# Kernel optimization log

Measured on AMD Instinct MI355X. Metric: run time of the kernel, lower is better.

## Reference

```python
import jax, jax.numpy as jnp
import numpy as np

T = 8          # num_timesteps
H = 8          # num_heads
D = 128        # lifting_dim
ROPE_BASE = 10000.0


def apply_time_only_rope(x, num_nodes, num_timesteps, base=ROPE_BASE):
    # x: [B, H, num_nodes*num_timesteps, d_head], time-major flattening
    B, Hh, S, dh = x.shape
    half = dh // 2
    times = jnp.arange(num_timesteps, dtype=jnp.float32)
    freqs = 1.0 / base ** (2.0 * jnp.arange(half, dtype=jnp.float32) / dh)
    angle = times[:, None] * freqs[None, :]                 # [T, half]
    positions = jnp.repeat(jnp.arange(num_timesteps), num_nodes)  # [S]
    cos_g = jnp.cos(angle)[positions]                       # [S, half]
    sin_g = jnp.sin(angle)[positions]
    t1 = x[..., 0::2]
    t2 = x[..., 1::2]
    r0 = t1 * cos_g - t2 * sin_g
    r1 = t1 * sin_g + t2 * cos_g
    return jnp.stack([r0, r1], axis=-1).reshape(x.shape)


def setup_inputs() -> dict:
    key = jax.random.key(0)
    ks = jax.random.split(key, 16)
    B_T, N, E = 32, 2048, 8192
    inp = {
        'x_0': jax.random.normal(ks[0], (B_T, N, D), jnp.float32),
        'edge_attr': jax.random.normal(ks[1], (B_T, E, D), jnp.float32),
        'q_data': jax.random.normal(ks[2], (B_T, N, D), jnp.float32),
    }
    def lin(k):
        kw, kb = jax.random.split(k)
        return (jax.random.normal(kw, (D, D), jnp.float32) * 0.02,
                jax.random.normal(kb, (D,), jnp.float32) * 0.02)
    inp['Wq'], inp['bq'] = lin(ks[3])
    inp['Wk0'], inp['bk0'] = lin(ks[4])
    inp['Wv0'], inp['bv0'] = lin(ks[5])
    inp['Wk1'], inp['bk1'] = lin(ks[6])
    inp['Wv1'], inp['bv1'] = lin(ks[7])
    inp['Wo'], inp['bo'] = lin(ks[8])
    return inp


def reference(x_0, edge_attr, q_data, Wq, bq, Wk0, bk0, Wv0, bv0, Wk1, bk1, Wv1, bv1, Wo, bo):
    B_T, N, d = x_0.shape
    B = B_T // T
    dh = d // H

    def flatten_st(a):  # [B*T, M, d] -> [B, T*M, d]
        return a.reshape(B, T * a.shape[1], d)

    qf = flatten_st(q_data) @ Wq.T + bq                     # [B, T*N, d]
    q = qf.reshape(B, H, N * T, dh)                         # faithful torch .view
    q = jax.nn.softmax(q, axis=-1)
    q = apply_time_only_rope(q, N, T)

    out = q
    for (feat, Wk, bk, Wv, bv) in ((x_0, Wk0, bk0, Wv0, bv0),
                                   (edge_attr, Wk1, bk1, Wv1, bv1)):
        M = feat.shape[1]
        hf = flatten_st(feat)                               # [B, T*M, d]
        k = (hf @ Wk.T + bk).reshape(B, H, M * T, dh)
        v = (hf @ Wv.T + bv).reshape(B, H, M * T, dh)
        k = apply_time_only_rope(k, M, T)
        k = jax.nn.softmax(k, axis=-1)
        k_cumsum = k.sum(axis=-2, keepdims=True)            # [B,H,1,dh]
        D_inv = 1.0 / jnp.maximum((q * k_cumsum).sum(axis=-1, keepdims=True), 1e-8)
        kv = jnp.einsum('bhsd,bhse->bhde', k, v)            # [B,H,dh,dh]
        out = q + jnp.einsum('bhsd,bhde->bhse', q, kv) * D_inv

    out = out.transpose(0, 2, 1, 3).reshape(B, N * T, d)
    out = out @ Wo.T + bo
    return out.reshape(B * T, N, d)                         # unflatten_spatiotemporal
```

## Files before the change

kernel.cpp:

```cpp
#include <hip/hip_runtime.h>
#include <hip/hip_bf16.h>
#include <math.h>


typedef __attribute__((ext_vector_type(8))) short short8;
typedef __attribute__((ext_vector_type(4))) float float4v;

#define LN1E4_OVER8 1.1512925464970229f

#define OFF_QWS   0
#define OFF_FRG_Q 4194304
#define OFF_FRG_O 4202496
#define OFF_BFRG  4210688
#define OFF_KV    4227072
#define OFF_KCS   4235264
#define OFF_PART  4235776

__device__ __forceinline__ unsigned short f2bf(float f) {
    __hip_bfloat16 h = __float2bfloat16(f);
    return *reinterpret_cast<unsigned short*>(&h);
}
__device__ __forceinline__ float bf2f(unsigned short s) {
    return __uint_as_float(((unsigned)s) << 16);
}
__device__ __forceinline__ unsigned pk2(float a, float b) {
    __hip_bfloat162 h = __float22bfloat162_rn(make_float2(a, b));
    return *reinterpret_cast<unsigned*>(&h);
}
__device__ __forceinline__ float frcp(float x) {
    return __builtin_amdgcn_rcpf(x);
}
template<int C> __device__ __forceinline__ float dppadd(float x) {
    int r = __builtin_amdgcn_update_dpp(0, __float_as_int(x), C, 0xF, 0xF, true);
    return x + __int_as_float(r);
}
__device__ __forceinline__ float sum16(float x) {
    x = dppadd<0xB1>(x);
    x = dppadd<0x4E>(x);
    x = dppadd<0x141>(x);
    x = dppadd<0x140>(x);
    return x;
}
__device__ __forceinline__ float qperm1(float x) {
    int r = __builtin_amdgcn_update_dpp(0, __float_as_int(x), 0xB1, 0xF, 0xF, true);
    return __int_as_float(r);
}

__global__ void k_prep(const float* __restrict__ Wq, const float* __restrict__ Wk1,
                       const float* __restrict__ Wv1, const float* __restrict__ Wo,
                       float* __restrict__ ws) {
    int i = blockIdx.x * 256 + threadIdx.x;
    if (i < 32768) {
        int j = i & 16383;
        int jE = j & 7, lane = (j >> 3) & 63, km = (j >> 9) & 3, cg = j >> 11;
        int n = cg * 16 + (lane & 15);
        int kk = km * 32 + (lane >> 4) * 8 + jE;
        const float* W = (i < 16384) ? Wq : Wo;
        unsigned short* dst = (unsigned short*)(ws + ((i < 16384) ? OFF_FRG_Q : OFF_FRG_O));
        dst[j] = f2bf(W[n * 128 + kk]);
    } else if (i < 65536) {
        int j = i - 32768;
        int jE = j & 7, lane = (j >> 3) & 63, km = (j >> 9) & 3, cg = j >> 11;
        int n = cg * 16 + (lane & 15);
        int k = km * 32 + (lane >> 4) * 8 + jE;
        float w = (cg < 8) ? Wk1[n * 128 + k] : Wv1[(n - 128) * 128 + k];
        ((unsigned short*)(ws + OFF_BFRG))[j] = f2bf(w);
    } else {
        int j = i - 65536;
        if (j < 8704) ws[OFF_KV + j] = 0.f;
    }
}

__global__ __launch_bounds__(256, 4) void k_main(const float* __restrict__ ea,
                                                 const float* __restrict__ bk,
                                                 const float* __restrict__ bv,
                                                 const float* __restrict__ qd,
                                                 const float* __restrict__ bq,
                                                 float* __restrict__ ws) {
    __shared__ __align__(16) char smem[40960];
    int t = threadIdx.x;
    int wave = t >> 6, lane = t & 63, quad = lane >> 4, n = lane & 15;
    int g = blockIdx.x;

    if (g % 5 == 4) {
        int blk = g / 5;
        unsigned short* aT = (unsigned short*)smem;
        unsigned* qws32 = (unsigned*)(ws + OFF_QWS);
        long base = (long)blk * 128;
        int b = blk >> 7;
        int h = (blk & 127) >> 4;
        int s0 = (blk & 15) * 1024;
        int t1 = (blk & 15) >> 1;

        const short8* fq = (const short8*)((const unsigned short*)(ws + OFF_FRG_Q));
        short8 Bf[2][4];
        #pragma unroll
        for (int ct = 0; ct < 2; ++ct)
            #pragma unroll
            for (int km = 0; km < 4; ++km)
                Bf[ct][km] = fq[((2 * wave + ct) * 4 + km) * 64 + lane];

        #pragma unroll
        for (int i = 0; i < 16; ++i) {
            int idx = i * 256 + t;
            int row = idx >> 5, c4 = idx & 31;
            float4 v = ((const float4*)qd)[(base + row) * 32 + c4];
            unsigned short* p = aT + row * 128 + (((c4 >> 1) ^ (row & 7)) << 3) + (c4 & 1) * 4;
            *(uint2*)p = make_uint2(pk2(v.x, v.y), pk2(v.z, v.w));
        }
        __syncthreads();

        float fr = __expf(-LN1E4_OVER8 * (float)(n >> 1));
        float sa, ca; __sincosf((float)t1 * fr, &sa, &ca);
        float sgn = (n & 1) ? sa : -sa;
        float bias0 = bq[(2 * wave) * 16 + n];
        float bias1 = bq[(2 * wave + 1) * 16 + n];

        #pragma unroll
        for (int rt = 0; rt < 8; ++rt) {
            float4v a0 = (float4v){0.f, 0.f, 0.f, 0.f};
            float4v a1 = (float4v){0.f, 0.f, 0.f, 0.f};
            int row = rt * 16 + n;
            __builtin_amdgcn_s_setprio(1);
            #pragma unroll
            for (int km = 0; km < 4; ++km) {
                short8 Af = *(const short8*)(aT + row * 128 + (((km * 4 + quad) ^ (n & 7)) << 3));
                a0 = __builtin_amdgcn_mfma_f32_16x16x32_bf16(Af, Bf[0][km], a0, 0, 0, 0);
                a1 = __builtin_amdgcn_mfma_f32_16x16x32_bf16(Af, Bf[1][km], a1, 0, 0, 0);
            }
            __builtin_amdgcn_s_setprio(0);
            #pragma unroll
            for (int ct = 0; ct < 2; ++ct) {
                int cg = 2 * wave + ct;
                float bias = ct ? bias1 : bias0;
                float4v x = ct ? a1 : a0;
                #pragma unroll
                for (int i = 0; i < 4; ++i) {
                    float e = __expf(x[i] + bias);
                    float q = e * frcp(sum16(e));
                    float r = fmaf(qperm1(q), sgn, q * ca);
                    unsigned pkd = ((unsigned)f2bf(qperm1(r)) << 16) | (unsigned)f2bf(r);
                    if ((n & 1) == 0) {
                        int sp = s0 + (rt * 16 + quad * 4 + i) * 8 + cg;
                        long qoff = ((long)(b * 8 + h) * 16384 + sp) * 16 + n;
                        qws32[qoff >> 1] = pkd;
                    }
                }
            }
        }
        return;
    }

    int blk = g - g / 5;
    unsigned short* aT = (unsigned short*)smem;
    unsigned short* kbuf = (unsigned short*)(smem + 32768) + wave * 1024;
    unsigned short* vbuf = kbuf + 512;
    long base = (long)blk * 128;
    int sl = (blk & 511) << 7;
    int t2 = (sl & 8191) >> 10;

    #pragma unroll
    for (int i = 0; i < 16; ++i) {
        int idx = i * 256 + t;
        int row = idx >> 5, c4 = idx & 31;
        float4 v = ((const float4*)ea)[(base + row) * 32 + c4];
        unsigned short* p = aT + row * 128 + (((c4 >> 1) ^ (row & 7)) << 3) + (c4 & 1) * 4;
        *(uint2*)p = make_uint2(pk2(v.x, v.y), pk2(v.z, v.w));
    }

    const short8* bfrag = (const short8*)((const unsigned short*)(ws + OFF_BFRG));
    short8 Bf[4][4];
    #pragma unroll
    for (int ct = 0; ct < 4; ++ct) {
        int cg = (ct < 2) ? (2 * wave + ct) : (8 + 2 * wave + (ct - 2));
        #pragma unroll
        for (int km = 0; km < 4; ++km)
            Bf[ct][km] = bfrag[(cg * 4 + km) * 64 + lane];
    }

    float bias[4];
    #pragma unroll
    for (int ct = 0; ct < 4; ++ct)
        bias[ct] = (ct < 2) ? bk[(2 * wave + ct) * 16 + n] : bv[(2 * wave + ct - 2) * 16 + n];
    float fr = __expf(-LN1E4_OVER8 * (float)(n >> 1));
    float sv, cvv; __sincosf((float)t2 * fr, &sv, &cvv);
    float sgn = (n & 1) ? sv : -sv;
    float kcsacc = 0.f;
    float4v kvacc = (float4v){0.f, 0.f, 0.f, 0.f};

    __syncthreads();

    #pragma unroll
    for (int rt = 0; rt < 8; ++rt) {
        float4v acc[4];
        #pragma unroll
        for (int ct = 0; ct < 4; ++ct) acc[ct] = (float4v){0.f, 0.f, 0.f, 0.f};

        int row = rt * 16 + n;
        short8 Af[4];
        #pragma unroll
        for (int km = 0; km < 4; ++km)
            Af[km] = *(const short8*)(aT + row * 128 + (((km * 4 + quad) ^ (n & 7)) << 3));
        __builtin_amdgcn_s_setprio(1);
        #pragma unroll
        for (int ct = 0; ct < 4; ++ct)
            #pragma unroll
            for (int km = 0; km < 4; ++km)
                acc[ct] = __builtin_amdgcn_mfma_f32_16x16x32_bf16(Af[km], Bf[ct][km], acc[ct], 0, 0, 0);
        __builtin_amdgcn_s_setprio(0);

        #pragma unroll
        for (int ct = 0; ct < 4; ++ct) {
            float x0 = acc[ct][0] + bias[ct];
            float x1 = acc[ct][1] + bias[ct];
            float x2 = acc[ct][2] + bias[ct];
            float x3 = acc[ct][3] + bias[ct];
            if (ct < 2) {
                x0 = fmaf(qperm1(x0), sgn, x0 * cvv); x1 = fmaf(qperm1(x1), sgn, x1 * cvv);
                x2 = fmaf(qperm1(x2), sgn, x2 * cvv); x3 = fmaf(qperm1(x3), sgn, x3 * cvv);
                x0 = __expf(x0); x1 = __expf(x1); x2 = __expf(x2); x3 = __expf(x3);
                x0 *= frcp(sum16(x0)); x1 *= frcp(sum16(x1));
                x2 *= frcp(sum16(x2)); x3 *= frcp(sum16(x3));
                kcsacc += x0 + x1 + x2 + x3;
            }
            unsigned short* dst = (ct < 2) ? kbuf : vbuf;
            int o = (ct & 1) * 16 + quad * 4;
            *(uint2*)(dst + n * 32 + (((o >> 3) ^ (n & 3)) << 3) + (o & 7)) =
                make_uint2(pk2(x0, x1), pk2(x2, x3));
        }

        asm volatile("s_waitcnt lgkmcnt(0)" ::: "memory");
        __builtin_amdgcn_sched_barrier(0);

        {
            int off = ((quad ^ (n & 3)) << 3);
            short8 Ak = *(const short8*)(kbuf + n * 32 + off);
            short8 Bv = *(const short8*)(vbuf + n * 32 + off);
            kvacc = __builtin_amdgcn_mfma_f32_16x16x32_bf16(Ak, Bv, kvacc, 0, 0, 0);
        }
    }

    kcsacc += __shfl_xor(kcsacc, 16); kcsacc += __shfl_xor(kcsacc, 32);
    float* part = ws + OFF_PART + ((long)blk * 4 + wave) * 272;
    #pragma unroll
    for (int r = 0; r < 4; ++r) part[(quad * 4 + r) * 16 + n] = kvacc[r];
    if (lane < 16) part[256 + n] = kcsacc;
}

__global__ void k_red(float* __restrict__ ws) {
    int blk = blockIdx.x, t = threadIdx.x;
    if (t >= 272) return;
    int bh = blk >> 3, g = blk & 7;
    const float* part = ws + OFF_PART + (long)bh * 256 * 272 + (long)g * 32 * 272 + t;
    float s = 0.f;
    #pragma unroll 8
    for (int i = 0; i < 32; ++i) s += part[(long)i * 272];
    float* dst = (t < 256) ? (ws + OFF_KV + bh * 256 + t)
                           : (ws + OFF_KCS + bh * 16 + (t - 256));
    atomicAdd(dst, s);
}

__global__ __launch_bounds__(256, 4) void k_out(const float* __restrict__ bo,
                                                float* __restrict__ ws,
                                                float* __restrict__ out) {
    __shared__ __align__(16) unsigned short tile[64 * 128];
    const unsigned short* qws16 = (const unsigned short*)(ws + OFF_QWS);
    int t = threadIdx.x, blk = blockIdx.x;
    int wave = t >> 6, lane = t & 63, quad = lane >> 4, n = lane & 15;
    int b = blk >> 8;
    int sp0 = (blk & 255) * 64;

    #pragma unroll
    for (int i = 0; i < 8; ++i) {
        int idx = i * 256 + t;
        int h = idx >> 8, rr = (idx >> 2) & 63, seg = idx & 3;
        uint2 u = *(const uint2*)(qws16 + ((long)(b * 8 + h) * 16384 + sp0 + rr) * 16 + seg * 4);
        unsigned short* p = tile + rr * 128 + (((h * 2 + (seg >> 1)) ^ (rr & 7)) << 3) + (seg & 1) * 4;
        *(uint2*)p = u;
    }

    short8 Bkv[2], Bden[2];
    #pragma unroll
    for (int ct = 0; ct < 2; ++ct) {
        int h = 2 * wave + ct;
        const float* kvp = ws + OFF_KV + (b * 8 + h) * 256;
        const float* ksp = ws + OFF_KCS + (b * 8 + h) * 16;
        short8 bk8 = {0, 0, 0, 0, 0, 0, 0, 0}, bd8 = {0, 0, 0, 0, 0, 0, 0, 0};
        bool act = (ct == 0) ? (quad < 2) : (quad >= 2);
        int kbase = (ct == 0) ? quad * 8 : (quad - 2) * 8;
        if (act) {
            #pragma unroll
            for (int jj = 0; jj < 8; ++jj) {
                bk8[jj] = (short)f2bf(kvp[(kbase + jj) * 16 + n]);
                bd8[jj] = (short)f2bf(ksp[kbase + jj]);
            }
        }
        Bkv[ct] = bk8; Bden[ct] = bd8;
    }
    const short8* fo = (const short8*)((const unsigned short*)(ws + OFF_FRG_O));
    short8 Bo[2][4];
    #pragma unroll
    for (int ct = 0; ct < 2; ++ct)
        #pragma unroll
        for (int km = 0; km < 4; ++km)
            Bo[ct][km] = fo[((2 * wave + ct) * 4 + km) * 64 + lane];
    __syncthreads();

    #pragma unroll
    for (int pass = 0; pass < 2; ++pass) {
        unsigned short fh[2][2][4];
        #pragma unroll
        for (int rtl = 0; rtl < 2; ++rtl) {
            int rt = pass * 2 + rtl;
            int row = rt * 16 + n;
            short8 Af = *(const short8*)(tile + row * 128 + (((wave * 4 + quad) ^ (n & 7)) << 3));
            float4v P0 = __builtin_amdgcn_mfma_f32_16x16x32_bf16(Af, Bkv[0], (float4v){0.f,0.f,0.f,0.f}, 0, 0, 0);
            float4v P1 = __builtin_amdgcn_mfma_f32_16x16x32_bf16(Af, Bkv[1], (float4v){0.f,0.f,0.f,0.f}, 0, 0, 0);
            float4v D0 = __builtin_amdgcn_mfma_f32_16x16x32_bf16(Af, Bden[0], (float4v){0.f,0.f,0.f,0.f}, 0, 0, 0);
            float4v D1 = __builtin_amdgcn_mfma_f32_16x16x32_bf16(Af, Bden[1], (float4v){0.f,0.f,0.f,0.f}, 0, 0, 0);
            #pragma unroll
            for (int ct = 0; ct < 2; ++ct) {
                int cg = 2 * wave + ct;
                float4v P = ct ? P1 : P0;
                float4v D = ct ? D1 : D0;
                #pragma unroll
                for (int i = 0; i < 4; ++i) {
                    int rw = rt * 16 + quad * 4 + i;
                    int col = cg * 16 + n;
                    float qv = bf2f(tile[rw * 128 + (((col >> 3) ^ (rw & 7)) << 3) + (col & 7)]);
                    float inv = frcp(fmaxf(D[i], 1e-8f));
                    fh[rtl][ct][i] = f2bf(fmaf(P[i], inv, qv));
                }
            }
        }
        __syncthreads();
        #pragma unroll
        for (int rtl = 0; rtl < 2; ++rtl)
            #pragma unroll
            for (int ct = 0; ct < 2; ++ct) {
                int cg = 2 * wave + ct;
                #pragma unroll
                for (int i = 0; i < 4; ++i) {
                    int rw = (pass * 2 + rtl) * 16 + quad * 4 + i;
                    int col = cg * 16 + n;
                    tile[rw * 128 + (((col >> 3) ^ (rw & 7)) << 3) + (col & 7)] = fh[rtl][ct][i];
                }
            }
    }
    __syncthreads();

    float bb0 = bo[(2 * wave) * 16 + n];
    float bb1 = bo[(2 * wave + 1) * 16 + n];
    #pragma unroll
    for (int rt = 0; rt < 4; ++rt) {
        float4v a0 = (float4v){0.f, 0.f, 0.f, 0.f};
        float4v a1 = (float4v){0.f, 0.f, 0.f, 0.f};
        int row = rt * 16 + n;
        #pragma unroll
        for (int km = 0; km < 4; ++km) {
            short8 Af = *(const short8*)(tile + row * 128 + (((km * 4 + quad) ^ (n & 7)) << 3));
            a0 = __builtin_amdgcn_mfma_f32_16x16x32_bf16(Af, Bo[0][km], a0, 0, 0, 0);
            a1 = __builtin_amdgcn_mfma_f32_16x16x32_bf16(Af, Bo[1][km], a1, 0, 0, 0);
        }
        #pragma unroll
        for (int ct = 0; ct < 2; ++ct) {
            int cg = 2 * wave + ct;
            float bb = ct ? bb1 : bb0;
            float4v a = ct ? a1 : a0;
            #pragma unroll
            for (int i = 0; i < 4; ++i) {
                float v = a[i] + bb;
                float pv = qperm1(v);
                if ((n & 1) == 0) {
                    long rg = (long)b * 16384 + sp0 + rt * 16 + quad * 4 + i;
                    *(float2*)(out + rg * 128 + cg * 16 + n) = make_float2(v, pv);
                }
            }
        }
    }
}

extern "C" void kernel_launch(void* const* d_in, const int* in_sizes, int n_in,
                              void* d_out, int out_size, void* d_ws, size_t ws_size,
                              hipStream_t stream) {
    (void)in_sizes; (void)n_in; (void)out_size; (void)ws_size;
    const float* edge = (const float*)d_in[1];
    const float* qd   = (const float*)d_in[2];
    const float* Wq   = (const float*)d_in[3];
    const float* bq   = (const float*)d_in[4];
    const float* Wk1  = (const float*)d_in[9];
    const float* bk1  = (const float*)d_in[10];
    const float* Wv1  = (const float*)d_in[11];
    const float* bv1  = (const float*)d_in[12];
    const float* Wo   = (const float*)d_in[13];
    const float* bo   = (const float*)d_in[14];
    float* ws  = (float*)d_ws;
    float* out = (float*)d_out;

    hipLaunchKernelGGL(k_prep, dim3(290),  dim3(256), 0, stream, Wq, Wk1, Wv1, Wo, ws);
    hipLaunchKernelGGL(k_main, dim3(2560), dim3(256), 0, stream, edge, bk1, bv1, qd, bq, ws);
    hipLaunchKernelGGL(k_red,  dim3(256),  dim3(320), 0, stream, ws);
    hipLaunchKernelGGL(k_out,  dim3(1024), dim3(256), 0, stream, bo, ws, out);
}
```

Before: 283.0 us.

## Halve k_main LDS tile for higher occupancy, widen k_red, load Q directly in k_out

k_main now stages its 128-row input in two 64-row halves, which cuts shared memory from 40KB to 24KB and raises the launch-bounds occupancy target from 4 to 6 blocks. k_red doubles its grid so each block sums 16 partials instead of 32. k_out no longer stages Q into LDS first: it reads MFMA A-fragments and the residual q values straight from global memory, and it drops the per-pass barrier. In exchange there is an extra barrier per half in k_main, register pressure is tighter under the higher occupancy bound, and k_out does more scattered global reads and issues more atomics.

```diff
diff --git a/kernel.cpp b/kernel.cpp
--- a/kernel.cpp
+++ b/kernel.cpp
@@ -71,13 +71,13 @@
     }
 }
 
-__global__ __launch_bounds__(256, 4) void k_main(const float* __restrict__ ea,
+__global__ __launch_bounds__(256, 6) void k_main(const float* __restrict__ ea,
                                                  const float* __restrict__ bk,
                                                  const float* __restrict__ bv,
                                                  const float* __restrict__ qd,
                                                  const float* __restrict__ bq,
                                                  float* __restrict__ ws) {
-    __shared__ __align__(16) char smem[40960];
+    __shared__ __align__(16) char smem[24576];
     int t = threadIdx.x;
     int wave = t >> 6, lane = t & 63, quad = lane >> 4, n = lane & 15;
     int g = blockIdx.x;
@@ -100,16 +100,6 @@
             for (int km = 0; km < 4; ++km)
                 Bf[ct][km] = fq[((2 * wave + ct) * 4 + km) * 64 + lane];
 
-        #pragma unroll
-        for (int i = 0; i < 16; ++i) {
-            int idx = i * 256 + t;
-            int row = idx >> 5, c4 = idx & 31;
-            float4 v = ((const float4*)qd)[(base + row) * 32 + c4];
-            unsigned short* p = aT + row * 128 + (((c4 >> 1) ^ (row & 7)) << 3) + (c4 & 1) * 4;
-            *(uint2*)p = make_uint2(pk2(v.x, v.y), pk2(v.z, v.w));
-        }
-        __syncthreads();
-
         float fr = __expf(-LN1E4_OVER8 * (float)(n >> 1));
         float sa, ca; __sincosf((float)t1 * fr, &sa, &ca);
         float sgn = (n & 1) ? sa : -sa;
@@ -117,33 +107,48 @@
         float bias1 = bq[(2 * wave + 1) * 16 + n];
 
         #pragma unroll
-        for (int rt = 0; rt < 8; ++rt) {
-            float4v a0 = (float4v){0.f, 0.f, 0.f, 0.f};
-            float4v a1 = (float4v){0.f, 0.f, 0.f, 0.f};
-            int row = rt * 16 + n;
-            __builtin_amdgcn_s_setprio(1);
-            #pragma unroll
-            for (int km = 0; km < 4; ++km) {
-                short8 Af = *(const short8*)(aT + row * 128 + (((km * 4 + quad) ^ (n & 7)) << 3));
-                a0 = __builtin_amdgcn_mfma_f32_16x16x32_bf16(Af, Bf[0][km], a0, 0, 0, 0);
-                a1 = __builtin_amdgcn_mfma_f32_16x16x32_bf16(Af, Bf[1][km], a1, 0, 0, 0);
-            }
-            __builtin_amdgcn_s_setprio(0);
-            #pragma unroll
-            for (int ct = 0; ct < 2; ++ct) {
-                int cg = 2 * wave + ct;
-                float bias = ct ? bias1 : bias0;
-                float4v x = ct ? a1 : a0;
+        for (int half = 0; half < 2; ++half) {
+            if (half) __syncthreads();
+            #pragma unroll
+            for (int i = 0; i < 8; ++i) {
+                int idx = i * 256 + t;
+                int row = idx >> 5, c4 = idx & 31;
+                float4 v = ((const float4*)qd)[(base + half * 64 + row) * 32 + c4];
+                unsigned short* p = aT + row * 128 + (((c4 >> 1) ^ (row & 7)) << 3) + (c4 & 1) * 4;
+                *(uint2*)p = make_uint2(pk2(v.x, v.y), pk2(v.z, v.w));
+            }
+            __syncthreads();
+
+            #pragma unroll
+            for (int rl = 0; rl < 4; ++rl) {
+                int rt = half * 4 + rl;
+                float4v a0 = (float4v){0.f, 0.f, 0.f, 0.f};
+                float4v a1 = (float4v){0.f, 0.f, 0.f, 0.f};
+                int row = rl * 16 + n;
+                __builtin_amdgcn_s_setprio(1);
                 #pragma unroll
-                for (int i = 0; i < 4; ++i) {
-                    float e = __expf(x[i] + bias);
-                    float q = e * frcp(sum16(e));
-                    float r = fmaf(qperm1(q), sgn, q * ca);
-                    unsigned pkd = ((unsigned)f2bf(qperm1(r)) << 16) | (unsigned)f2bf(r);
-                    if ((n & 1) == 0) {
-                        int sp = s0 + (rt * 16 + quad * 4 + i) * 8 + cg;
-                        long qoff = ((long)(b * 8 + h) * 16384 + sp) * 16 + n;
-                        qws32[qoff >> 1] = pkd;
+                for (int km = 0; km < 4; ++km) {
+                    short8 Af = *(const short8*)(aT + row * 128 + (((km * 4 + quad) ^ (n & 7)) << 3));
+                    a0 = __builtin_amdgcn_mfma_f32_16x16x32_bf16(Af, Bf[0][km], a0, 0, 0, 0);
+                    a1 = __builtin_amdgcn_mfma_f32_16x16x32_bf16(Af, Bf[1][km], a1, 0, 0, 0);
+                }
+                __builtin_amdgcn_s_setprio(0);
+                #pragma unroll
+                for (int ct = 0; ct < 2; ++ct) {
+                    int cg = 2 * wave + ct;
+                    float bias = ct ? bias1 : bias0;
+                    float4v x = ct ? a1 : a0;
+                    #pragma unroll
+                    for (int i = 0; i < 4; ++i) {
+                        float e = __expf(x[i] + bias);
+                        float q = e * frcp(sum16(e));
+                        float r = fmaf(qperm1(q), sgn, q * ca);
+                        unsigned pkd = ((unsigned)f2bf(qperm1(r)) << 16) | (unsigned)f2bf(r);
+                        if ((n & 1) == 0) {
+                            int sp = s0 + (rt * 16 + quad * 4 + i) * 8 + cg;
+                            long qoff = ((long)(b * 8 + h) * 16384 + sp) * 16 + n;
+                            qws32[qoff >> 1] = pkd;
+                        }
                     }
                 }
             }
@@ -153,20 +158,11 @@
 
     int blk = g - g / 5;
     unsigned short* aT = (unsigned short*)smem;
-    unsigned short* kbuf = (unsigned short*)(smem + 32768) + wave * 1024;
+    unsigned short* kbuf = (unsigned short*)(smem + 16384) + wave * 1024;
     unsigned short* vbuf = kbuf + 512;
     long base = (long)blk * 128;
     int sl = (blk & 511) << 7;
     int t2 = (sl & 8191) >> 10;
-
-    #pragma unroll
-    for (int i = 0; i < 16; ++i) {
-        int idx = i * 256 + t;
-        int row = idx >> 5, c4 = idx & 31;
-        float4 v = ((const float4*)ea)[(base + row) * 32 + c4];
-        unsigned short* p = aT + row * 128 + (((c4 >> 1) ^ (row & 7)) << 3) + (c4 & 1) * 4;
-        *(uint2*)p = make_uint2(pk2(v.x, v.y), pk2(v.z, v.w));
-    }
 
     const short8* bfrag = (const short8*)((const unsigned short*)(ws + OFF_BFRG));
     short8 Bf[4][4];
@@ -188,55 +184,67 @@
     float kcsacc = 0.f;
     float4v kvacc = (float4v){0.f, 0.f, 0.f, 0.f};
 
-    __syncthreads();
-
-    #pragma unroll
-    for (int rt = 0; rt < 8; ++rt) {
-        float4v acc[4];
-        #pragma unroll
-        for (int ct = 0; ct < 4; ++ct) acc[ct] = (float4v){0.f, 0.f, 0.f, 0.f};
-
-        int row = rt * 16 + n;
-        short8 Af[4];
-        #pragma unroll
-        for (int km = 0; km < 4; ++km)
-            Af[km] = *(const short8*)(aT + row * 128 + (((km * 4 + quad) ^ (n & 7)) << 3));
-        __builtin_amdgcn_s_setprio(1);
-        #pragma unroll
-        for (int ct = 0; ct < 4; ++ct)
+    #pragma unroll
+    for (int half = 0; half < 2; ++half) {
+        if (half) __syncthreads();
+        #pragma unroll
+        for (int i = 0; i < 8; ++i) {
+            int idx = i * 256 + t;
+            int row = idx >> 5, c4 = idx & 31;
+            float4 v = ((const float4*)ea)[(base + half * 64 + row) * 32 + c4];
+            unsigned short* p = aT + row * 128 + (((c4 >> 1) ^ (row & 7)) << 3) + (c4 & 1) * 4;
+            *(uint2*)p = make_uint2(pk2(v.x, v.y), pk2(v.z, v.w));
+        }
+        __syncthreads();
+
+        #pragma unroll
+        for (int rl = 0; rl < 4; ++rl) {
+            float4v acc[4];
+            #pragma unroll
+            for (int ct = 0; ct < 4; ++ct) acc[ct] = (float4v){0.f, 0.f, 0.f, 0.f};
+
+            int row = rl * 16 + n;
+            short8 Af[4];
             #pragma unroll
             for (int km = 0; km < 4; ++km)
-                acc[ct] = __builtin_amdgcn_mfma_f32_16x16x32_bf16(Af[km], Bf[ct][km], acc[ct], 0, 0, 0);
-        __builtin_amdgcn_s_setprio(0);
-
-        #pragma unroll
-        for (int ct = 0; ct < 4; ++ct) {
-            float x0 = acc[ct][0] + bias[ct];
-            float x1 = acc[ct][1] + bias[ct];
-            float x2 = acc[ct][2] + bias[ct];
-            float x3 = acc[ct][3] + bias[ct];
-            if (ct < 2) {
-                x0 = fmaf(qperm1(x0), sgn, x0 * cvv); x1 = fmaf(qperm1(x1), sgn, x1 * cvv);
-                x2 = fmaf(qperm1(x2), sgn, x2 * cvv); x3 = fmaf(qperm1(x3), sgn, x3 * cvv);
-                x0 = __expf(x0); x1 = __expf(x1); x2 = __expf(x2); x3 = __expf(x3);
-                x0 *= frcp(sum16(x0)); x1 *= frcp(sum16(x1));
-                x2 *= frcp(sum16(x2)); x3 *= frcp(sum16(x3));
-                kcsacc += x0 + x1 + x2 + x3;
-            }
-            unsigned short* dst = (ct < 2) ? kbuf : vbuf;
-            int o = (ct & 1) * 16 + quad * 4;
-            *(uint2*)(dst + n * 32 + (((o >> 3) ^ (n & 3)) << 3) + (o & 7)) =
-                make_uint2(pk2(x0, x1), pk2(x2, x3));
-        }
-
-        asm volatile("s_waitcnt lgkmcnt(0)" ::: "memory");
-        __builtin_amdgcn_sched_barrier(0);
-
-        {
-            int off = ((quad ^ (n & 3)) << 3);
-            short8 Ak = *(const short8*)(kbuf + n * 32 + off);
-            short8 Bv = *(const short8*)(vbuf + n * 32 + off);
-            kvacc = __builtin_amdgcn_mfma_f32_16x16x32_bf16(Ak, Bv, kvacc, 0, 0, 0);
+                Af[km] = *(const short8*)(aT + row * 128 + (((km * 4 + quad) ^ (n & 7)) << 3));
+            __builtin_amdgcn_s_setprio(1);
+            #pragma unroll
+            for (int ct = 0; ct < 4; ++ct)
+                #pragma unroll
+                for (int km = 0; km < 4; ++km)
+                    acc[ct] = __builtin_amdgcn_mfma_f32_16x16x32_bf16(Af[km], Bf[ct][km], acc[ct], 0, 0, 0);
+            __builtin_amdgcn_s_setprio(0);
+
+            #pragma unroll
+            for (int ct = 0; ct < 4; ++ct) {
+                float x0 = acc[ct][0] + bias[ct];
+                float x1 = acc[ct][1] + bias[ct];
+                float x2 = acc[ct][2] + bias[ct];
+                float x3 = acc[ct][3] + bias[ct];
+                if (ct < 2) {
+                    x0 = fmaf(qperm1(x0), sgn, x0 * cvv); x1 = fmaf(qperm1(x1), sgn, x1 * cvv);
+                    x2 = fmaf(qperm1(x2), sgn, x2 * cvv); x3 = fmaf(qperm1(x3), sgn, x3 * cvv);
+                    x0 = __expf(x0); x1 = __expf(x1); x2 = __expf(x2); x3 = __expf(x3);
+                    x0 *= frcp(sum16(x0)); x1 *= frcp(sum16(x1));
+                    x2 *= frcp(sum16(x2)); x3 *= frcp(sum16(x3));
+                    kcsacc += x0 + x1 + x2 + x3;
+                }
+                unsigned short* dst = (ct < 2) ? kbuf : vbuf;
+                int o = (ct & 1) * 16 + quad * 4;
+                *(uint2*)(dst + n * 32 + (((o >> 3) ^ (n & 3)) << 3) + (o & 7)) =
+                    make_uint2(pk2(x0, x1), pk2(x2, x3));
+            }
+
+            asm volatile("s_waitcnt lgkmcnt(0)" ::: "memory");
+            __builtin_amdgcn_sched_barrier(0);
+
+            {
+                int off = ((quad ^ (n & 3)) << 3);
+                short8 Ak = *(const short8*)(kbuf + n * 32 + off);
+                short8 Bv = *(const short8*)(vbuf + n * 32 + off);
+                kvacc = __builtin_amdgcn_mfma_f32_16x16x32_bf16(Ak, Bv, kvacc, 0, 0, 0);
+            }
         }
     }
 
@@ -250,11 +258,11 @@
 __global__ void k_red(float* __restrict__ ws) {
     int blk = blockIdx.x, t = threadIdx.x;
     if (t >= 272) return;
-    int bh = blk >> 3, g = blk & 7;
-    const float* part = ws + OFF_PART + (long)bh * 256 * 272 + (long)g * 32 * 272 + t;
+    int bh = blk >> 4, gg = blk & 15;
+    const float* part = ws + OFF_PART + (long)bh * 256 * 272 + (long)gg * 16 * 272 + t;
     float s = 0.f;
     #pragma unroll 8
-    for (int i = 0; i < 32; ++i) s += part[(long)i * 272];
+    for (int i = 0; i < 16; ++i) s += part[(long)i * 272];
     float* dst = (t < 256) ? (ws + OFF_KV + bh * 256 + t)
                            : (ws + OFF_KCS + bh * 16 + (t - 256));
     atomicAdd(dst, s);
@@ -270,15 +278,6 @@
     int b = blk >> 8;
     int sp0 = (blk & 255) * 64;
 
-    #pragma unroll
-    for (int i = 0; i < 8; ++i) {
-        int idx = i * 256 + t;
-        int h = idx >> 8, rr = (idx >> 2) & 63, seg = idx & 3;
-        uint2 u = *(const uint2*)(qws16 + ((long)(b * 8 + h) * 16384 + sp0 + rr) * 16 + seg * 4);
-        unsigned short* p = tile + rr * 128 + (((h * 2 + (seg >> 1)) ^ (rr & 7)) << 3) + (seg & 1) * 4;
-        *(uint2*)p = u;
-    }
-
     short8 Bkv[2], Bden[2];
     #pragma unroll
     for (int ct = 0; ct < 2; ++ct) {
@@ -304,49 +303,43 @@
         #pragma unroll
         for (int km = 0; km < 4; ++km)
             Bo[ct][km] = fo[((2 * wave + ct) * 4 + km) * 64 + lane];
-    __syncthreads();
-
-    #pragma unroll
-    for (int pass = 0; pass < 2; ++pass) {
-        unsigned short fh[2][2][4];
-        #pragma unroll
-        for (int rtl = 0; rtl < 2; ++rtl) {
-            int rt = pass * 2 + rtl;
-            int row = rt * 16 + n;
-            short8 Af = *(const short8*)(tile + row * 128 + (((wave * 4 + quad) ^ (n & 7)) << 3));
-            float4v P0 = __builtin_amdgcn_mfma_f32_16x16x32_bf16(Af, Bkv[0], (float4v){0.f,0.f,0.f,0.f}, 0, 0, 0);
-            float4v P1 = __builtin_amdgcn_mfma_f32_16x16x32_bf16(Af, Bkv[1], (float4v){0.f,0.f,0.f,0.f}, 0, 0, 0);
-            float4v D0 = __builtin_amdgcn_mfma_f32_16x16x32_bf16(Af, Bden[0], (float4v){0.f,0.f,0.f,0.f}, 0, 0, 0);
-            float4v D1 = __builtin_amdgcn_mfma_f32_16x16x32_bf16(Af, Bden[1], (float4v){0.f,0.f,0.f,0.f}, 0, 0, 0);
-            #pragma unroll
-            for (int ct = 0; ct < 2; ++ct) {
-                int cg = 2 * wave + ct;
-                float4v P = ct ? P1 : P0;
-                float4v D = ct ? D1 : D0;
-                #pragma unroll
-                for (int i = 0; i < 4; ++i) {
-                    int rw = rt * 16 + quad * 4 + i;
-                    int col = cg * 16 + n;
-                    float qv = bf2f(tile[rw * 128 + (((col >> 3) ^ (rw & 7)) << 3) + (col & 7)]);
-                    float inv = frcp(fmaxf(D[i], 1e-8f));
-                    fh[rtl][ct][i] = f2bf(fmaf(P[i], inv, qv));
-                }
-            }
-        }
-        __syncthreads();
-        #pragma unroll
-        for (int rtl = 0; rtl < 2; ++rtl)
-            #pragma unroll
-            for (int ct = 0; ct < 2; ++ct) {
-                int cg = 2 * wave + ct;
-                #pragma unroll
-                for (int i = 0; i < 4; ++i) {
-                    int rw = (pass * 2 + rtl) * 16 + quad * 4 + i;
-                    int col = cg * 16 + n;
-                    tile[rw * 128 + (((col >> 3) ^ (rw & 7)) << 3) + (col & 7)] = fh[rtl][ct][i];
-                }
-            }
-    }
+
+    unsigned short fh[4][2][4];
+    int hA = 2 * wave + (quad >> 1);
+    const unsigned short* qbase = qws16 + ((long)(b * 8 + hA) * 16384 + sp0) * 16 + (quad & 1) * 8;
+    #pragma unroll
+    for (int rt = 0; rt < 4; ++rt) {
+        short8 Af = *(const short8*)(qbase + (long)(rt * 16 + n) * 16);
+        float4v P0 = __builtin_amdgcn_mfma_f32_16x16x32_bf16(Af, Bkv[0], (float4v){0.f,0.f,0.f,0.f}, 0, 0, 0);
+        float4v P1 = __builtin_amdgcn_mfma_f32_16x16x32_bf16(Af, Bkv[1], (float4v){0.f,0.f,0.f,0.f}, 0, 0, 0);
+        float4v D0 = __builtin_amdgcn_mfma_f32_16x16x32_bf16(Af, Bden[0], (float4v){0.f,0.f,0.f,0.f}, 0, 0, 0);
+        float4v D1 = __builtin_amdgcn_mfma_f32_16x16x32_bf16(Af, Bden[1], (float4v){0.f,0.f,0.f,0.f}, 0, 0, 0);
+        #pragma unroll
+        for (int ct = 0; ct < 2; ++ct) {
+            int cg = 2 * wave + ct;
+            float4v P = ct ? P1 : P0;
+            float4v D = ct ? D1 : D0;
+            #pragma unroll
+            for (int i = 0; i < 4; ++i) {
+                int rw = rt * 16 + quad * 4 + i;
+                float qv = bf2f(qws16[((long)(b * 8 + cg) * 16384 + sp0 + rw) * 16 + n]);
+                float inv = frcp(fmaxf(D[i], 1e-8f));
+                fh[rt][ct][i] = f2bf(fmaf(P[i], inv, qv));
+            }
+        }
+    }
+    #pragma unroll
+    for (int rt = 0; rt < 4; ++rt)
+        #pragma unroll
+        for (int ct = 0; ct < 2; ++ct) {
+            int cg = 2 * wave + ct;
+            #pragma unroll
+            for (int i = 0; i < 4; ++i) {
+                int rw = rt * 16 + quad * 4 + i;
+                int col = cg * 16 + n;
+                tile[rw * 128 + (((col >> 3) ^ (rw & 7)) << 3) + (col & 7)] = fh[rt][ct][i];
+            }
+        }
     __syncthreads();
 
     float bb0 = bo[(2 * wave) * 16 + n];
@@ -399,6 +392,6 @@
 
     hipLaunchKernelGGL(k_prep, dim3(290),  dim3(256), 0, stream, Wq, Wk1, Wv1, Wo, ws);
     hipLaunchKernelGGL(k_main, dim3(2560), dim3(256), 0, stream, edge, bk1, bv1, qd, bq, ws);
-    hipLaunchKernelGGL(k_red,  dim3(256),  dim3(320), 0, stream, ws);
+    hipLaunchKernelGGL(k_red,  dim3(512),  dim3(320), 0, stream, ws);
     hipLaunchKernelGGL(k_out,  dim3(1024), dim3(256), 0, stream, bo, ws, out);
 }
```

After: 441.4 us. 56.0% more time.
